# Performance work log

Hardware: AMD Instinct MI355X
Metric: run time of the kernel (lower is better)

Reference implementation:

```python
import jax, jax.numpy as jnp
import numpy as np

N = 10000      # nodes
E = 320000     # edges (avg degree 32)
IN = 512       # in_channels
OUT = 128      # out_channels
H = 4          # in_head
C1 = 2 * OUT   # per-head hidden channels of conv1 (256)
NEG_SLOPE = 0.2


def setup_inputs() -> dict:
    key = jax.random.key(0)
    ks = jax.random.split(key, 12)
    x = jax.random.normal(ks[0], (N, IN), dtype=jnp.float32)
    edge_index = jax.random.randint(ks[1], (2, E), 0, N, dtype=jnp.int64)
    def glorot(k, shape):
        lim = np.sqrt(6.0 / (shape[0] + shape[-1])).astype(np.float32)
        return jax.random.uniform(k, shape, jnp.float32, -lim, lim)
    # conv1: GATv2Conv(IN -> C1 per head, heads=H)
    Wl1 = glorot(ks[2], (IN, H * C1))
    Wr1 = glorot(ks[3], (IN, H * C1))
    att1 = glorot(ks[4], (H, C1))
    b1 = jnp.zeros((H * C1,), jnp.float32)
    # conv2: GATv2Conv(H*C1 -> OUT, heads=1)
    Wl2 = glorot(ks[5], (H * C1, OUT))
    Wr2 = glorot(ks[6], (H * C1, OUT))
    att2 = glorot(ks[7], (1, OUT))
    b2 = jnp.zeros((OUT,), jnp.float32)
    return {"x": x, "edge_index": edge_index, "Wl1": Wl1, "Wr1": Wr1,
            "att1": att1, "b1": b1, "Wl2": Wl2, "Wr2": Wr2,
            "att2": att2, "b2": b2}


def gatv2_conv(x, src, dst, Wl, Wr, att, b, heads, ch):
    # x: [N, F_in]; src/dst: [E] (message src -> dst, softmax over dst)
    n = x.shape[0]
    xl = (x @ Wl).reshape(n, heads, ch)   # source-side projection
    xr = (x @ Wr).reshape(n, heads, ch)   # target-side projection
    # per-edge GATv2 score: att . LeakyReLU(xl_j + xr_i)   [E, H]
    e = jax.nn.leaky_relu(xl[src] + xr[dst], NEG_SLOPE)    # [E, H, C]
    s = jnp.einsum('ehc,hc->eh', e, att)                   # [E, H]
    # segment softmax over incoming edges of each dst node
    smax = jax.lax.stop_gradient(jax.ops.segment_max(s, dst, num_segments=n))
    ex = jnp.exp(s - smax[dst])
    denom = jax.ops.segment_sum(ex, dst, num_segments=n)
    alpha = ex / denom[dst]                                # [E, H]
    # weighted scatter-add of source messages
    out = jax.ops.segment_sum(alpha[:, :, None] * xl[src], dst, num_segments=n)
    return out.reshape(n, heads * ch) + b                  # concat heads + bias


def reference(x, edge_index, Wl1, Wr1, att1, b1, Wl2, Wr2, att2, b2):
    src, dst = edge_index[0], edge_index[1]
    h = gatv2_conv(x, src, dst, Wl1, Wr1, att1, b1, H, C1)
    h = jax.nn.relu(h)                                     # [N, H*C1]
    out = gatv2_conv(h, src, dst, Wl2, Wr2, att2, b2, 1, OUT)
    return out                                             # [N, OUT]
```

## Files before the change

kernel.cpp:

```cpp
#include <hip/hip_runtime.h>
#include <cfloat>

#define N_NODES 10000
#define N_EDGES 320000
#define IN_F    512
#define F1      1024
#define OUT_F   128
#define NEG     0.2f
#define BUCKET  128

typedef __attribute__((ext_vector_type(8))) short bf16x8;
typedef __attribute__((ext_vector_type(4))) float f32x4;
typedef __attribute__((ext_vector_type(2))) float f32x2;
typedef __attribute__((ext_vector_type(4))) unsigned int u32x4;
typedef __attribute__((ext_vector_type(4))) unsigned short u16x4;

__device__ __forceinline__ float lrelu(float v) { return fmaxf(v, NEG * v); }

__device__ __forceinline__ unsigned short f2bf(float f) {
    unsigned u = __float_as_uint(f);
    u += 0x7fff + ((u >> 16) & 1);
    return (unsigned short)(u >> 16);
}
__device__ __forceinline__ float bf2f(unsigned short h) {
    return __uint_as_float(((unsigned)h) << 16);
}
__device__ __forceinline__ void u2f2(unsigned u, float& e0, float& e1) {
    e0 = __uint_as_float(u << 16);
    e1 = __uint_as_float(u & 0xffff0000u);
}

__device__ __forceinline__ float rsum16(float x) {
    x += __int_as_float(__builtin_amdgcn_update_dpp(0, __float_as_int(x), 0x121, 0xF, 0xF, false));
    x += __int_as_float(__builtin_amdgcn_update_dpp(0, __float_as_int(x), 0x122, 0xF, 0xF, false));
    x += __int_as_float(__builtin_amdgcn_update_dpp(0, __float_as_int(x), 0x124, 0xF, 0xF, false));
    x += __int_as_float(__builtin_amdgcn_update_dpp(0, __float_as_int(x), 0x128, 0xF, 0xF, false));
    return x;
}

__device__ __forceinline__ void gld_lds16(const void* g, void* l) {
    __builtin_amdgcn_global_load_lds(
        (const __attribute__((address_space(1))) unsigned int*)g,
        (__attribute__((address_space(3))) unsigned int*)l, 16, 0, 0);
}

#define PB_X  2500
#define PB_S  3750
#define PB_W1 4774
#define PB_END 5030

__device__ __forceinline__ void wt_body(const float* __restrict__ Wa,
                                        const float* __restrict__ Wb,
                                        unsigned short* __restrict__ tbf,
                                        int K, int NS, int n0, int k0, int t,
                                        float (*tile)[33]) {
    int j = t & 31;
    const float* W = (n0 < NS) ? Wa : Wb;
    int nb = (n0 < NS) ? n0 : n0 - NS;
#pragma unroll
    for (int r = 0; r < 4; ++r) {
        int kl = (t >> 5) + r * 8;
        tile[kl][j] = W[(size_t)(k0 + kl) * NS + nb + j];
    }
    __syncthreads();
#pragma unroll
    for (int r = 0; r < 4; ++r) {
        int nl = (t >> 5) + r * 8;
        tbf[(size_t)(n0 + nl) * K + k0 + j] = f2bf(tile[j][nl]);
    }
}

__global__ __launch_bounds__(256) void k_prep(const float* __restrict__ x,
                                              unsigned short* __restrict__ xbf,
                                              const int* __restrict__ ei,
                                              int* __restrict__ cnt,
                                              int* __restrict__ esrc,
                                              const float* __restrict__ Wl1,
                                              const float* __restrict__ Wr1,
                                              unsigned short* __restrict__ w1bf,
                                              const float* __restrict__ Wl2,
                                              const float* __restrict__ Wr2,
                                              unsigned short* __restrict__ w2bf) {
    __shared__ float tile[32][33];
    int bid = blockIdx.x, t = threadIdx.x;
    if (bid < PB_X) {
        int i = bid * 2048 + t * 8;
        f32x4 v0 = __builtin_nontemporal_load((const f32x4*)(x + i));
        f32x4 v1 = __builtin_nontemporal_load((const f32x4*)(x + i + 4));
        ushort4 h0, h1;
        h0.x = f2bf(v0.x); h0.y = f2bf(v0.y); h0.z = f2bf(v0.z); h0.w = f2bf(v0.w);
        h1.x = f2bf(v1.x); h1.y = f2bf(v1.y); h1.z = f2bf(v1.z); h1.w = f2bf(v1.w);
        *(ushort4*)(xbf + i) = h0;
        *(ushort4*)(xbf + i + 4) = h1;
    } else if (bid < PB_S) {
        int e = (bid - PB_X) * 256 + t;
        if (e < N_EDGES) {
            int d = ei[N_EDGES + e];
            int pos = atomicAdd(&cnt[d], 1);
            if (pos < BUCKET) esrc[(size_t)d * BUCKET + pos] = ei[e];
        }
    } else if (bid < PB_W1) {
        int local = bid - PB_S;
        wt_body(Wl1, Wr1, w1bf, IN_F, F1, (local & 63) * 32, (local >> 6) * 32, t, tile);
    } else {
        int local = bid - PB_W1;
        wt_body(Wl2, Wr2, w2bf, F1, OUT_F, (local & 7) * 32, (local >> 3) * 32, t, tile);
    }
}

__global__ __launch_bounds__(256) void k_sort(const int* __restrict__ cnt,
                                              int* __restrict__ esrc) {
    int t = threadIdx.x;
    int w = t >> 6, lane = t & 63;
    int nd = blockIdx.x * 4 + w;
    if (nd >= N_NODES) return;
    int deg = min(cnt[nd], 64);
    int p0 = nd * BUCKET;
    int v = (lane < deg) ? esrc[p0 + lane] : 0x7fffffff;
#pragma unroll
    for (int k = 2; k <= 64; k <<= 1) {
#pragma unroll
        for (int j = k >> 1; j > 0; j >>= 1) {
            int other = __shfl_xor(v, j);
            bool dir = ((lane & k) == 0);
            bool lower = ((lane & j) == 0);
            int mn = min(v, other), mx = max(v, other);
            v = (lower == dir) ? mn : mx;
        }
    }
    if (lane < deg) esrc[p0 + lane] = v;
}

template<int BM> struct GemmSmem {
    union {
        struct { short As[BM * 32]; short Bs[128 * 32]; } st;
        unsigned short ct[BM * 136];
    };
};

template<int BM, int WR, int WC>
__global__ __launch_bounds__(256) void gemm_mfma(
        const unsigned short* __restrict__ A,
        const unsigned short* __restrict__ B,
        unsigned short* __restrict__ Cl, unsigned short* __restrict__ Cr,
        int M, int K, int NSPLIT) {
    constexpr int NI = BM / (16 * WR);
    constexpr int NJ = 128 / (16 * WC);
    __shared__ __align__(16) GemmSmem<BM> sm;
    int t = threadIdx.x;
    int lane = t & 63, w = t >> 6;
    int row0 = blockIdx.y * BM;
    int n0 = blockIdx.x * 128;
    int wr0 = (w / WC) * (NI * 16);
    int wc0 = (w % WC) * (NJ * 16);
    int q = lane >> 4, md = lane & 15;
    int srow = t >> 2;
    int skoff = (t & 3) * 8;

    f32x4 acc[NI][NJ];
#pragma unroll
    for (int i = 0; i < NI; ++i)
#pragma unroll
        for (int j = 0; j < NJ; ++j)
#pragma unroll
            for (int r = 0; r < 4; ++r) acc[i][j][r] = 0.f;

    for (int k0 = 0; k0 < K; k0 += 32) {
        __syncthreads();
#pragma unroll
        for (int is = 0; is < BM / 64; ++is) {
            int gr = row0 + is * 64 + srow;
            if (gr < M)
                gld_lds16(A + (size_t)gr * K + k0 + skoff,
                          &sm.st.As[(is * 64 + (t >> 6) * 16) * 32]);
        }
#pragma unroll
        for (int is = 0; is < 2; ++is) {
            int gn = n0 + is * 64 + srow;
            gld_lds16(B + (size_t)gn * K + k0 + skoff,
                      &sm.st.Bs[(is * 64 + (t >> 6) * 16) * 32]);
        }
        __syncthreads();

        bf16x8 av[NI], bv[NJ];
#pragma unroll
        for (int i = 0; i < NI; ++i)
            av[i] = *(const bf16x8*)&sm.st.As[(wr0 + i * 16 + md) * 32 + q * 8];
#pragma unroll
        for (int j = 0; j < NJ; ++j)
            bv[j] = *(const bf16x8*)&sm.st.Bs[(wc0 + j * 16 + md) * 32 + q * 8];
#pragma unroll
        for (int i = 0; i < NI; ++i)
#pragma unroll
            for (int j = 0; j < NJ; ++j)
                acc[i][j] = __builtin_amdgcn_mfma_f32_16x16x32_bf16(av[i], bv[j], acc[i][j], 0, 0, 0);
    }

    __syncthreads();
#pragma unroll
    for (int i = 0; i < NI; ++i)
#pragma unroll
        for (int j = 0; j < NJ; ++j)
#pragma unroll
            for (int r = 0; r < 4; ++r)
                sm.ct[(wr0 + i * 16 + q * 4 + r) * 136 + wc0 + j * 16 + md] =
                    f2bf(acc[i][j][r]);
    __syncthreads();
    unsigned short* C = (n0 < NSPLIT) ? Cl : Cr;
    int cc0 = (n0 < NSPLIT) ? n0 : n0 - NSPLIT;
    for (int idx = t; idx < BM * 16; idx += 256) {
        int row = idx >> 4, seg = idx & 15;
        if (row0 + row < M) {
            bf16x8 val = *(const bf16x8*)&sm.ct[row * 136 + seg * 8];
            *(bf16x8*)(C + (size_t)(row0 + row) * NSPLIT + cc0 + seg * 8) = val;
        }
    }
}

__global__ __launch_bounds__(256) void k_fused1(const unsigned short* __restrict__ xlbf,
                                                const unsigned short* __restrict__ xrbf,
                                                const int* __restrict__ cnt,
                                                const int* __restrict__ esrc,
                                                const float* __restrict__ att,
                                                const float* __restrict__ bias,
                                                unsigned short* __restrict__ hb) {
    int t = threadIdx.x;
    int w = t >> 6, lane = t & 63;
    int ni = w >> 1;
    int ww = w & 1;
    int nd = blockIdx.x * 2 + ni;
    int head = lane >> 4, sub = lane & 15;
    int ch = head * 256 + sub * 16;

    __shared__ float slx[4][4];
    __shared__ float4 sacc4[2][4][64];

    float4 r0, r1, r2, r3;
    {
        const u32x4* prx = (const u32x4*)(xrbf + (size_t)nd * F1 + ch);
        u32x4 xa = __builtin_nontemporal_load(prx);
        u32x4 xb = __builtin_nontemporal_load(prx + 1);
        u2f2(xa.x, r0.x, r0.y); u2f2(xa.y, r0.z, r0.w);
        u2f2(xa.z, r1.x, r1.y); u2f2(xa.w, r1.z, r1.w);
        u2f2(xb.x, r2.x, r2.y); u2f2(xb.y, r2.z, r2.w);
        u2f2(xb.z, r3.x, r3.y); u2f2(xb.w, r3.z, r3.w);
    }
    const float4* pa = (const float4*)(att + ch);
    float4 a0 = pa[0], a1 = pa[1], a2 = pa[2], a3 = pa[3];

    int deg = min(cnt[nd], BUCKET);
    int p0 = nd * BUCKET;
    int dege = min(deg, 64);
    int bkt = (lane < dege) ? esrc[p0 + lane] : 0;

    float l = 0.f;
    float4 acc0 = make_float4(0.f, 0.f, 0.f, 0.f);
    float4 acc1 = acc0, acc2 = acc0, acc3 = acc0;

    auto edge_body = [&](uint4 ca, uint4 cb) {
        float4 c0, c1, c2, c3;
        u2f2(ca.x, c0.x, c0.y); u2f2(ca.y, c0.z, c0.w);
        u2f2(ca.z, c1.x, c1.y); u2f2(ca.w, c1.z, c1.w);
        u2f2(cb.x, c2.x, c2.y); u2f2(cb.y, c2.z, c2.w);
        u2f2(cb.z, c3.x, c3.y); u2f2(cb.w, c3.z, c3.w);
        float u;
        float sl0, sa0, sl1, sa1, sl2, sa2, sl3, sa3;
        u = c0.x + r0.x; sl0 = a0.x * u;           sa0 = a0.x * fabsf(u);
        u = c0.y + r0.y; sl0 = fmaf(a0.y, u, sl0); sa0 = fmaf(a0.y, fabsf(u), sa0);
        u = c0.z + r0.z; sl0 = fmaf(a0.z, u, sl0); sa0 = fmaf(a0.z, fabsf(u), sa0);
        u = c0.w + r0.w; sl0 = fmaf(a0.w, u, sl0); sa0 = fmaf(a0.w, fabsf(u), sa0);
        u = c1.x + r1.x; sl1 = a1.x * u;           sa1 = a1.x * fabsf(u);
        u = c1.y + r1.y; sl1 = fmaf(a1.y, u, sl1); sa1 = fmaf(a1.y, fabsf(u), sa1);
        u = c1.z + r1.z; sl1 = fmaf(a1.z, u, sl1); sa1 = fmaf(a1.z, fabsf(u), sa1);
        u = c1.w + r1.w; sl1 = fmaf(a1.w, u, sl1); sa1 = fmaf(a1.w, fabsf(u), sa1);
        u = c2.x + r2.x; sl2 = a2.x * u;           sa2 = a2.x * fabsf(u);
        u = c2.y + r2.y; sl2 = fmaf(a2.y, u, sl2); sa2 = fmaf(a2.y, fabsf(u), sa2);
        u = c2.z + r2.z; sl2 = fmaf(a2.z, u, sl2); sa2 = fmaf(a2.z, fabsf(u), sa2);
        u = c2.w + r2.w; sl2 = fmaf(a2.w, u, sl2); sa2 = fmaf(a2.w, fabsf(u), sa2);
        u = c3.x + r3.x; sl3 = a3.x * u;           sa3 = a3.x * fabsf(u);
        u = c3.y + r3.y; sl3 = fmaf(a3.y, u, sl3); sa3 = fmaf(a3.y, fabsf(u), sa3);
        u = c3.z + r3.z; sl3 = fmaf(a3.z, u, sl3); sa3 = fmaf(a3.z, fabsf(u), sa3);
        u = c3.w + r3.w; sl3 = fmaf(a3.w, u, sl3); sa3 = fmaf(a3.w, fabsf(u), sa3);
        float sl = (sl0 + sl1) + (sl2 + sl3);
        float sa = (sa0 + sa1) + (sa2 + sa3);
        float s = rsum16(fmaf(0.6f, sl, 0.4f * sa));
        s = fminf(fmaxf(s, -60.f), 60.f);
        float al = __expf(s);
        l += al;
        acc0.x = fmaf(al, c0.x, acc0.x);
        acc0.y = fmaf(al, c0.y, acc0.y);
        acc0.z = fmaf(al, c0.z, acc0.z);
        acc0.w = fmaf(al, c0.w, acc0.w);
        acc1.x = fmaf(al, c1.x, acc1.x);
        acc1.y = fmaf(al, c1.y, acc1.y);
        acc1.z = fmaf(al, c1.z, acc1.z);
        acc1.w = fmaf(al, c1.w, acc1.w);
        acc2.x = fmaf(al, c2.x, acc2.x);
        acc2.y = fmaf(al, c2.y, acc2.y);
        acc2.z = fmaf(al, c2.z, acc2.z);
        acc2.w = fmaf(al, c2.w, acc2.w);
        acc3.x = fmaf(al, c3.x, acc3.x);
        acc3.y = fmaf(al, c3.y, acc3.y);
        acc3.z = fmaf(al, c3.z, acc3.z);
        acc3.w = fmaf(al, c3.w, acc3.w);
    };

    int idx = ww;
    uint4 ua, ub;
    if (idx < dege) {
        int sn = __shfl(bkt, idx);
        const uint4* pv = (const uint4*)(xlbf + (size_t)sn * F1 + ch);
        ua = pv[0]; ub = pv[1];
    }
    for (; idx < dege; idx += 2) {
        uint4 ca = ua, cb = ub;
        int nidx = idx + 2;
        if (nidx < dege) {
            int sn = __shfl(bkt, nidx);
            const uint4* pv = (const uint4*)(xlbf + (size_t)sn * F1 + ch);
            ua = pv[0]; ub = pv[1];
        }
        edge_body(ca, cb);
    }
    for (int p = p0 + 64 + ww; p < p0 + deg; p += 2) {
        const uint4* pv = (const uint4*)(xlbf + (size_t)esrc[p] * F1 + ch);
        edge_body(pv[0], pv[1]);
    }

    if (sub == 0) slx[w][head] = l;
    if (ww == 1) {
        sacc4[ni][0][lane] = acc0;
        sacc4[ni][1][lane] = acc1;
        sacc4[ni][2][lane] = acc2;
        sacc4[ni][3][lane] = acc3;
    }
    __syncthreads();
    if (ww == 0) {
        float L = l + slx[w ^ 1][head];
        float invL = (L > 0.f) ? 1.f / L : 0.f;
        const float4* pb = (const float4*)(bias + ch);
        size_t base = (size_t)nd * F1 + ch;
        float4 aa[4] = {acc0, acc1, acc2, acc3};
#pragma unroll
        for (int j = 0; j < 4; ++j) {
            float4 pt = sacc4[ni][j][lane];
            float4 b4 = pb[j];
            u16x4 hv;
            hv.x = f2bf(fmaxf(fmaf(aa[j].x + pt.x, invL, b4.x), 0.f));
            hv.y = f2bf(fmaxf(fmaf(aa[j].y + pt.y, invL, b4.y), 0.f));
            hv.z = f2bf(fmaxf(fmaf(aa[j].z + pt.z, invL, b4.z), 0.f));
            hv.w = f2bf(fmaxf(fmaf(aa[j].w + pt.w, invL, b4.w), 0.f));
            __builtin_nontemporal_store(hv, (u16x4*)(hb + base + j * 4));
        }
    }
}

__global__ __launch_bounds__(256) void k_fused2(const unsigned short* __restrict__ xlbf,
                                                const unsigned short* __restrict__ xrbf,
                                                const int* __restrict__ cnt,
                                                const int* __restrict__ esrc,
                                                const float* __restrict__ att,
                                                const float* __restrict__ bias,
                                                float* __restrict__ out) {
    int t = threadIdx.x;
    int w = t >> 6, lane = t & 63;
    int nd = blockIdx.x * 4 + w;
    int g = lane >> 4, sub = lane & 15;
    int ch = sub * 8;

    __shared__ float slx2[4][4];
    __shared__ float sacc2[4][4][132];

    float r[8], a[8];
    {
        u32x4 u = __builtin_nontemporal_load(
            (const u32x4*)(xrbf + (size_t)nd * OUT_F + ch));
        u2f2(u.x, r[0], r[1]); u2f2(u.y, r[2], r[3]);
        u2f2(u.z, r[4], r[5]); u2f2(u.w, r[6], r[7]);
        float4 q0 = *(const float4*)(att + ch);
        float4 q1 = *(const float4*)(att + ch + 4);
        a[0] = q0.x; a[1] = q0.y; a[2] = q0.z; a[3] = q0.w;
        a[4] = q1.x; a[5] = q1.y; a[6] = q1.z; a[7] = q1.w;
    }
    int deg = min(cnt[nd], BUCKET);
    int p0 = nd * BUCKET;
    int p1 = p0 + deg;

    float l = 0.f;
    float acc[8] = {};
    uint4 cur, nxt;
    {
        int p = p0 + g;
        if (p < p1)     cur = *(const uint4*)(xlbf + (size_t)esrc[p] * OUT_F + ch);
        if (p + 4 < p1) nxt = *(const uint4*)(xlbf + (size_t)esrc[p + 4] * OUT_F + ch);
    }
    for (int p = p0 + g; p < p1; p += 4) {
        uint4 c = cur;
        cur = nxt;
        if (p + 8 < p1) nxt = *(const uint4*)(xlbf + (size_t)esrc[p + 8] * OUT_F + ch);
        float v[8];
        u2f2(c.x, v[0], v[1]); u2f2(c.y, v[2], v[3]);
        u2f2(c.z, v[4], v[5]); u2f2(c.w, v[6], v[7]);
        float uu;
        float slA, saA, slB, saB;
        uu = v[0] + r[0]; slA = a[0] * uu;           saA = a[0] * fabsf(uu);
        uu = v[1] + r[1]; slA = fmaf(a[1], uu, slA); saA = fmaf(a[1], fabsf(uu), saA);
        uu = v[2] + r[2]; slA = fmaf(a[2], uu, slA); saA = fmaf(a[2], fabsf(uu), saA);
        uu = v[3] + r[3]; slA = fmaf(a[3], uu, slA); saA = fmaf(a[3], fabsf(uu), saA);
        uu = v[4] + r[4]; slB = a[4] * uu;           saB = a[4] * fabsf(uu);
        uu = v[5] + r[5]; slB = fmaf(a[5], uu, slB); saB = fmaf(a[5], fabsf(uu), saB);
        uu = v[6] + r[6]; slB = fmaf(a[6], uu, slB); saB = fmaf(a[6], fabsf(uu), saB);
        uu = v[7] + r[7]; slB = fmaf(a[7], uu, slB); saB = fmaf(a[7], fabsf(uu), saB);
        float s = rsum16(fmaf(0.6f, slA + slB, 0.4f * (saA + saB)));
        s = fminf(fmaxf(s, -60.f), 60.f);
        float al = __expf(s);
        l += al;
#pragma unroll
        for (int k = 0; k < 8; ++k) acc[k] = fmaf(al, v[k], acc[k]);
    }

    if (sub == 0) slx2[w][g] = l;
    float4 v0 = make_float4(acc[0], acc[1], acc[2], acc[3]);
    float4 v1 = make_float4(acc[4], acc[5], acc[6], acc[7]);
    *(float4*)&sacc2[w][g][ch] = v0;
    *(float4*)&sacc2[w][g][ch + 4] = v1;
    __syncthreads();
    float L = slx2[w][0] + slx2[w][1] + slx2[w][2] + slx2[w][3];
    float invL = (L > 0.f) ? 1.f / L : 0.f;
    int c2 = lane * 2;
    float o0 = sacc2[w][0][c2] + sacc2[w][1][c2] + sacc2[w][2][c2] + sacc2[w][3][c2];
    float o1 = sacc2[w][0][c2 + 1] + sacc2[w][1][c2 + 1] + sacc2[w][2][c2 + 1] + sacc2[w][3][c2 + 1];
    float2 bf = *(const float2*)(bias + c2);
    f32x2 o;
    o.x = fmaf(o0, invL, bf.x);
    o.y = fmaf(o1, invL, bf.y);
    __builtin_nontemporal_store(o, (f32x2*)(out + (size_t)nd * OUT_F + c2));
}

extern "C" void kernel_launch(void* const* d_in, const int* in_sizes, int n_in,
                              void* d_out, int out_size, void* d_ws, size_t ws_size,
                              hipStream_t stream) {
    const float* x    = (const float*)d_in[0];
    const int*   ei   = (const int*)d_in[1];
    const float* Wl1  = (const float*)d_in[2];
    const float* Wr1  = (const float*)d_in[3];
    const float* att1 = (const float*)d_in[4];
    const float* b1   = (const float*)d_in[5];
    const float* Wl2  = (const float*)d_in[6];
    const float* Wr2  = (const float*)d_in[7];
    const float* att2 = (const float*)d_in[8];
    const float* b2   = (const float*)d_in[9];
    float* out = (float*)d_out;

    unsigned short* us = (unsigned short*)d_ws;
    unsigned short* xl1bf = us;
    unsigned short* xr1bf = xl1bf + (size_t)N_NODES * F1;
    unsigned short* xl2bf = xr1bf + (size_t)N_NODES * F1;
    unsigned short* xr2bf = xl2bf + (size_t)N_NODES * OUT_F;
    unsigned short* hb   = xr2bf + (size_t)N_NODES * OUT_F;
    unsigned short* xbf  = hb + (size_t)N_NODES * F1;
    unsigned short* w1bf = xbf + (size_t)N_NODES * IN_F;
    unsigned short* w2bf = w1bf + (size_t)2048 * IN_F;
    int* cnt   = (int*)(w2bf + (size_t)256 * F1);
    int* esrc  = cnt + (N_NODES + 16);

    hipMemsetAsync(cnt, 0, sizeof(int) * N_NODES, stream);
    k_prep<<<PB_END, 256, 0, stream>>>(x, xbf, ei, cnt, esrc,
                                       Wl1, Wr1, w1bf,
                                       Wl2, Wr2, w2bf);

    k_sort<<<(N_NODES + 3) / 4, 256, 0, stream>>>(cnt, esrc);

    gemm_mfma<128, 2, 2><<<dim3(16, (N_NODES + 127) / 128), 256, 0, stream>>>(
        xbf, w1bf, xl1bf, xr1bf, N_NODES, IN_F, F1);

    k_fused1<<<N_NODES / 2, 256, 0, stream>>>(xl1bf, xr1bf, cnt, esrc, att1, b1, hb);

    gemm_mfma<64, 1, 4><<<dim3(2, (N_NODES + 63) / 64), 256, 0, stream>>>(
        hb, w2bf, xl2bf, xr2bf, N_NODES, F1, OUT_F);

    k_fused2<<<N_NODES / 4, 256, 0, stream>>>(xl2bf, xr2bf, cnt, esrc, att2, b2, out);
}
```

Before: 267.2 us.

## Fuse edge-source bitonic sort into conv1 aggregation and retile second GEMM

Removes the standalone k_sort launch and runs the per-node bitonic sort of source indices inside k_fused1, right after the bucket is loaded into registers. The sorted order is no longer written back, so k_fused2 now walks unsorted edge lists, which may hurt its gather locality. The GEMM template gains a BN parameter, and the second projection GEMM uses 64x64 tiles, doubling the block count for better occupancy. The hidden-activation store in k_fused1 becomes a regular store instead of a nontemporal one, so the next GEMM may find hb in cache.

```diff
diff --git a/kernel.cpp b/kernel.cpp
--- a/kernel.cpp
+++ b/kernel.cpp
@@ -13,7 +13,6 @@
 typedef __attribute__((ext_vector_type(4))) float f32x4;
 typedef __attribute__((ext_vector_type(2))) float f32x2;
 typedef __attribute__((ext_vector_type(4))) unsigned int u32x4;
-typedef __attribute__((ext_vector_type(4))) unsigned short u16x4;
 
 __device__ __forceinline__ float lrelu(float v) { return fmaxf(v, NEG * v); }
 
@@ -108,49 +107,26 @@
     }
 }
 
-__global__ __launch_bounds__(256) void k_sort(const int* __restrict__ cnt,
-                                              int* __restrict__ esrc) {
-    int t = threadIdx.x;
-    int w = t >> 6, lane = t & 63;
-    int nd = blockIdx.x * 4 + w;
-    if (nd >= N_NODES) return;
-    int deg = min(cnt[nd], 64);
-    int p0 = nd * BUCKET;
-    int v = (lane < deg) ? esrc[p0 + lane] : 0x7fffffff;
-#pragma unroll
-    for (int k = 2; k <= 64; k <<= 1) {
-#pragma unroll
-        for (int j = k >> 1; j > 0; j >>= 1) {
-            int other = __shfl_xor(v, j);
-            bool dir = ((lane & k) == 0);
-            bool lower = ((lane & j) == 0);
-            int mn = min(v, other), mx = max(v, other);
-            v = (lower == dir) ? mn : mx;
-        }
-    }
-    if (lane < deg) esrc[p0 + lane] = v;
-}
-
-template<int BM> struct GemmSmem {
+template<int BM, int BN> struct GemmSmem {
     union {
-        struct { short As[BM * 32]; short Bs[128 * 32]; } st;
-        unsigned short ct[BM * 136];
+        struct { short As[BM * 32]; short Bs[BN * 32]; } st;
+        unsigned short ct[BM * (BN + 8)];
     };
 };
 
-template<int BM, int WR, int WC>
+template<int BM, int BN, int WR, int WC>
 __global__ __launch_bounds__(256) void gemm_mfma(
         const unsigned short* __restrict__ A,
         const unsigned short* __restrict__ B,
         unsigned short* __restrict__ Cl, unsigned short* __restrict__ Cr,
         int M, int K, int NSPLIT) {
     constexpr int NI = BM / (16 * WR);
-    constexpr int NJ = 128 / (16 * WC);
-    __shared__ __align__(16) GemmSmem<BM> sm;
+    constexpr int NJ = BN / (16 * WC);
+    __shared__ __align__(16) GemmSmem<BM, BN> sm;
     int t = threadIdx.x;
     int lane = t & 63, w = t >> 6;
     int row0 = blockIdx.y * BM;
-    int n0 = blockIdx.x * 128;
+    int n0 = blockIdx.x * BN;
     int wr0 = (w / WC) * (NI * 16);
     int wc0 = (w % WC) * (NJ * 16);
     int q = lane >> 4, md = lane & 15;
@@ -175,7 +151,7 @@
                           &sm.st.As[(is * 64 + (t >> 6) * 16) * 32]);
         }
 #pragma unroll
-        for (int is = 0; is < 2; ++is) {
+        for (int is = 0; is < BN / 64; ++is) {
             int gn = n0 + is * 64 + srow;
             gld_lds16(B + (size_t)gn * K + k0 + skoff,
                       &sm.st.Bs[(is * 64 + (t >> 6) * 16) * 32]);
@@ -203,15 +179,16 @@
         for (int j = 0; j < NJ; ++j)
 #pragma unroll
             for (int r = 0; r < 4; ++r)
-                sm.ct[(wr0 + i * 16 + q * 4 + r) * 136 + wc0 + j * 16 + md] =
+                sm.ct[(wr0 + i * 16 + q * 4 + r) * (BN + 8) + wc0 + j * 16 + md] =
                     f2bf(acc[i][j][r]);
     __syncthreads();
     unsigned short* C = (n0 < NSPLIT) ? Cl : Cr;
     int cc0 = (n0 < NSPLIT) ? n0 : n0 - NSPLIT;
-    for (int idx = t; idx < BM * 16; idx += 256) {
-        int row = idx >> 4, seg = idx & 15;
+    constexpr int SEGS = BN / 8;
+    for (int idx = t; idx < BM * SEGS; idx += 256) {
+        int row = idx / SEGS, seg = idx % SEGS;
         if (row0 + row < M) {
-            bf16x8 val = *(const bf16x8*)&sm.ct[row * 136 + seg * 8];
+            bf16x8 val = *(const bf16x8*)&sm.ct[row * (BN + 8) + seg * 8];
             *(bf16x8*)(C + (size_t)(row0 + row) * NSPLIT + cc0 + seg * 8) = val;
         }
     }
@@ -251,7 +228,22 @@
     int deg = min(cnt[nd], BUCKET);
     int p0 = nd * BUCKET;
     int dege = min(deg, 64);
-    int bkt = (lane < dege) ? esrc[p0 + lane] : 0;
+    int bkt;
+    {
+        int sv = (lane < dege) ? esrc[p0 + lane] : 0x7fffffff;
+#pragma unroll
+        for (int k = 2; k <= 64; k <<= 1) {
+#pragma unroll
+            for (int j = k >> 1; j > 0; j >>= 1) {
+                int other = __shfl_xor(sv, j);
+                bool dir = ((lane & k) == 0);
+                bool lower = ((lane & j) == 0);
+                int mn = min(sv, other), mx = max(sv, other);
+                sv = (lower == dir) ? mn : mx;
+            }
+        }
+        bkt = sv;
+    }
 
     float l = 0.f;
     float4 acc0 = make_float4(0.f, 0.f, 0.f, 0.f);
@@ -345,12 +337,12 @@
         for (int j = 0; j < 4; ++j) {
             float4 pt = sacc4[ni][j][lane];
             float4 b4 = pb[j];
-            u16x4 hv;
+            ushort4 hv;
             hv.x = f2bf(fmaxf(fmaf(aa[j].x + pt.x, invL, b4.x), 0.f));
             hv.y = f2bf(fmaxf(fmaf(aa[j].y + pt.y, invL, b4.y), 0.f));
             hv.z = f2bf(fmaxf(fmaf(aa[j].z + pt.z, invL, b4.z), 0.f));
             hv.w = f2bf(fmaxf(fmaf(aa[j].w + pt.w, invL, b4.w), 0.f));
-            __builtin_nontemporal_store(hv, (u16x4*)(hb + base + j * 4));
+            *(ushort4*)(hb + base + j * 4) = hv;
         }
     }
 }
@@ -469,14 +461,12 @@
                                        Wl1, Wr1, w1bf,
                                        Wl2, Wr2, w2bf);
 
-    k_sort<<<(N_NODES + 3) / 4, 256, 0, stream>>>(cnt, esrc);
-
-    gemm_mfma<128, 2, 2><<<dim3(16, (N_NODES + 127) / 128), 256, 0, stream>>>(
+    gemm_mfma<128, 128, 2, 2><<<dim3(16, (N_NODES + 127) / 128), 256, 0, stream>>>(
         xbf, w1bf, xl1bf, xr1bf, N_NODES, IN_F, F1);
 
     k_fused1<<<N_NODES / 2, 256, 0, stream>>>(xl1bf, xr1bf, cnt, esrc, att1, b1, hb);
 
-    gemm_mfma<64, 1, 4><<<dim3(2, (N_NODES + 63) / 64), 256, 0, stream>>>(
+    gemm_mfma<64, 64, 2, 2><<<dim3(4, (N_NODES + 63) / 64), 256, 0, stream>>>(
         hb, w2bf, xl2bf, xr2bf, N_NODES, F1, OUT_F);
 
     k_fused2<<<N_NODES / 4, 256, 0, stream>>>(xl2bf, xr2bf, cnt, esrc, att2, b2, out);
```

Measured after the change: 253.5 us. -5.1%, faster.
